# Optimization experiments

Measured on AMD Instinct MI355X. Metric: run time of the kernel, lower is better.

The kernel has to match this reference:

```python
import jax, jax.numpy as jnp
import numpy as np

HID = 64; H = 2; D = 32; L = 2; G = 64; F_IN = 771
NA = 120000; NE = 60000; E0 = 1500000; E1 = 1000000; E2 = 1000000


def _seg_mean(x, seg, n):
    s = jax.ops.segment_sum(x, seg, num_segments=n)
    c = jax.ops.segment_sum(jnp.ones((x.shape[0], 1), x.dtype), seg, num_segments=n)
    return s / jnp.maximum(c, 1.0)


def setup_inputs() -> dict:
    ks = jax.random.split(jax.random.key(0), 32)
    r = lambda i, s: 0.02 * jax.random.normal(ks[i], s, jnp.float32)
    z = lambda s: jnp.zeros(s, jnp.float32)
    inp = {}
    inp['x_argument'] = jax.random.normal(ks[0], (NA, F_IN), jnp.float32)
    inp['x_evidence'] = jax.random.normal(ks[1], (NE, F_IN), jnp.float32)
    inp['Win'] = r(2, (2, F_IN, HID)); inp['b_in'] = z((2, HID))
    inp['Wk'] = r(3, (L, 2, HID, HID)); inp['bk'] = z((L, 2, HID))
    inp['Wq'] = r(4, (L, 2, HID, HID)); inp['bq'] = z((L, 2, HID))
    inp['Wv'] = r(5, (L, 2, HID, HID)); inp['bv'] = z((L, 2, HID))
    inp['Wa'] = r(6, (L, 2, HID, HID)); inp['ba'] = z((L, 2, HID))
    inp['skip'] = jnp.ones((L, 2), jnp.float32)
    inp['Watt'] = r(7, (L, 3, H, D, D)); inp['Wmsg'] = r(8, (L, 3, H, D, D))
    inp['prel'] = jnp.ones((L, 3, H), jnp.float32)
    inp['Wnews'] = r(9, (384, HID)); inp['bnews'] = z((HID,))
    inp['Wdeb'] = r(10, (HID, HID)); inp['bdeb'] = z((HID,))
    inp['Wqm'] = r(11, (HID, HID)); inp['bqm'] = z((HID,))
    inp['Wkm'] = r(12, (HID, HID)); inp['bkm'] = z((HID,))
    inp['Wvm'] = r(13, (HID, HID)); inp['bvm'] = z((HID,))
    inp['Wom'] = r(14, (HID, HID)); inp['bom'] = z((HID,))
    inp['Wc1'] = r(15, (2 * HID, 64)); inp['bc1'] = z((64,))
    inp['Wc2'] = r(16, (64, 1)); inp['bc2'] = z((1,))
    inp['e0_src'] = jax.random.randint(ks[17], (E0,), 0, NA)
    inp['e0_dst'] = jax.random.randint(ks[18], (E0,), 0, NA)
    inp['e1_src'] = jax.random.randint(ks[19], (E1,), 0, NE)
    inp['e1_dst'] = jax.random.randint(ks[20], (E1,), 0, NA)
    inp['e2_src'] = jax.random.randint(ks[21], (E2,), 0, NA)
    inp['e2_dst'] = jax.random.randint(ks[22], (E2,), 0, NE)
    inp['batch_arg'] = jnp.sort(jax.random.randint(ks[23], (NA,), 0, G))
    return inp


def reference(x_argument, x_evidence, Win, b_in, Wk, bk, Wq, bq, Wv, bv, Wa, ba,
              skip, Watt, Wmsg, prel, Wnews, bnews, Wdeb, bdeb,
              Wqm, bqm, Wkm, bkm, Wvm, bvm, Wom, bom, Wc1, bc1, Wc2, bc2,
              e0_src, e0_dst, e1_src, e1_dst, e2_src, e2_dst, batch_arg):
    # Claim embedding from RAW features (slice 384:768), pooled per graph.
    claim_raw = _seg_mean(x_argument[:, 384:768], batch_arg, G)
    # Per-node-type input projection + ReLU. type 0 = argument, 1 = evidence.
    xs = [jax.nn.relu(x_argument @ Win[0] + b_in[0]),
          jax.nn.relu(x_evidence @ Win[1] + b_in[1])]
    # (src_type, dst_type, src_idx, dst_idx) for each heterogeneous edge type.
    edges = [(0, 0, e0_src, e0_dst), (1, 0, e1_src, e1_dst), (0, 1, e2_src, e2_dst)]
    scale = 1.0 / jnp.sqrt(jnp.float32(D))
    for l in range(L):  # HGTConv stack
        Kt = [(xs[t] @ Wk[l, t] + bk[l, t]).reshape(-1, H, D) for t in range(2)]
        Qt = [(xs[t] @ Wq[l, t] + bq[l, t]).reshape(-1, H, D) for t in range(2)]
        Vt = [(xs[t] @ Wv[l, t] + bv[l, t]).reshape(-1, H, D) for t in range(2)]
        buf = {0: [], 1: []}
        for e, (s, d, src, dst) in enumerate(edges):
            k2 = jnp.einsum('ehd,hdf->ehf', Kt[s][src], Watt[l, e])  # relation key transform
            v2 = jnp.einsum('ehd,hdf->ehf', Vt[s][src], Wmsg[l, e])  # relation msg transform
            sc = (Qt[d][dst] * k2).sum(-1) * prel[l, e] * scale      # (E, H)
            buf[d].append((sc, dst, v2))
        new_xs = []
        for d in range(2):
            n = xs[d].shape[0]
            sc = jnp.concatenate([b[0] for b in buf[d]], 0)
            dst = jnp.concatenate([b[1] for b in buf[d]], 0)
            v2 = jnp.concatenate([b[2] for b in buf[d]], 0)
            # segment softmax over all incoming edges of each destination node
            m = jax.ops.segment_max(sc, dst, num_segments=n)
            ex = jnp.exp(sc - m[dst])
            den = jax.ops.segment_sum(ex, dst, num_segments=n)
            alpha = ex / den[dst]
            agg = jax.ops.segment_sum(alpha[..., None] * v2, dst, num_segments=n).reshape(n, HID)
            out = jax.nn.gelu(agg, approximate=False) @ Wa[l, d] + ba[l, d]
            beta = jax.nn.sigmoid(skip[l, d])
            new_xs.append(beta * out + (1.0 - beta) * xs[d])
        xs = new_xs
    graph_emb = _seg_mean(xs[0], batch_arg, G)
    eF = claim_raw @ Wnews + bnews          # (G, HID)
    g = graph_emb @ Wdeb + bdeb             # (G, HID)
    # MultiheadAttention with query len 1 and key len 1: softmax over a single
    # key is identically 1, so attn_out == out_proj(v_proj(g)) exactly
    # (Wqm/bqm/Wkm/bkm receive exactly zero gradient, matching torch).
    v = g @ Wvm + bvm
    attn_out = v @ Wom + bom
    h = jax.nn.relu(jnp.concatenate([g, attn_out], -1) @ Wc1 + bc1)  # dropout is eval-mode identity
    return h @ Wc2 + bc2  # (G, 1)
```

## Files before the change

### kernel.cpp

```cpp
#include <hip/hip_runtime.h>
#include <math.h>

#define N0 120000
#define N1 60000
#define E0N 1500000
#define E1N 1000000
#define E2N 1000000
#define FIN 771
#define NG 64
#define KSTEPS_IN 25

#define GB0 ((N0 + 127) / 128)
#define GB1 ((N1 + 127) / 128)
#define AB0 ((N0 + 3) / 4)
#define AB1 ((N1 + 3) / 4)
#define SB0 ((N0 + 1023) / 1024)
#define SB1 ((N1 + 1023) / 1024)

#define Q0O   ((size_t)0)
#define KV00O ((size_t)N0 * 64)
#define KV02O ((size_t)N0 * 192)
#define Q1O   ((size_t)N0 * 320)
#define KV11O ((size_t)N0 * 320 + (size_t)N1 * 64)

typedef __attribute__((ext_vector_type(8))) short short8;
typedef __attribute__((ext_vector_type(4))) float f32x4;
typedef float f32x4u __attribute__((ext_vector_type(4), aligned(4)));
typedef __attribute__((ext_vector_type(4))) unsigned short ushort4v;
typedef unsigned short ushort;

__device__ __forceinline__ float gelu_f(float v) {
    return 0.5f * v * (1.f + erff(v * 0.70710678118654752f));
}
__device__ __forceinline__ ushort f2b(float f) {
    union { float f; unsigned u; } v; v.f = f;
    unsigned u = v.u;
    return (ushort)((u + 0x7FFFu + ((u >> 16) & 1u)) >> 16);
}
__device__ __forceinline__ float lo16(unsigned u) {
    union { unsigned x; float f; } v; v.x = u << 16; return v.f;
}
__device__ __forceinline__ float hi16(unsigned u) {
    union { unsigned x; float f; } v; v.x = u & 0xFFFF0000u; return v.f;
}
__device__ __forceinline__ int asi(float f) { union { float f; int i; } v; v.f = f; return v.i; }
__device__ __forceinline__ float asf(int i) { union { int i; float f; } v; v.i = i; return v.f; }

__global__ __launch_bounds__(256) void in_proj_all(
    const float* __restrict__ xa, const float* __restrict__ xe,
    const ushort* __restrict__ Wpin, const float* __restrict__ b_in,
    float* __restrict__ xs0, float* __restrict__ xs1)
{
    const int bx = blockIdx.x;
    const int type = (bx >= GB0) ? 1 : 0;
    const float* __restrict__ x = type ? xe : xa;
    const int nrows = type ? N1 : N0;
    const ushort* __restrict__ Wp = Wpin + (type ? (size_t)KSTEPS_IN * 2048 : 0);
    const float* __restrict__ bias = b_in + type * 64;
    float* __restrict__ out = type ? xs1 : xs0;

    const int tid = threadIdx.x, w = tid >> 6, lane = tid & 63;
    const int r0 = (type ? bx - GB0 : bx) * 128 + w * 32;

    const int rA = min(r0 + (lane & 15), nrows - 1);
    const int rB = min(r0 + 16 + (lane & 15), nrows - 1);
    const float* __restrict__ xA = x + (size_t)rA * FIN + (lane >> 4) * 8;
    const float* __restrict__ xB = x + (size_t)rB * FIN + (lane >> 4) * 8;

    f32x4 acc[2][4] = {};
    f32x4u cA0 = *(const f32x4u*)xA;
    f32x4u cA1 = *(const f32x4u*)(xA + 4);
    f32x4u cB0 = *(const f32x4u*)xB;
    f32x4u cB1 = *(const f32x4u*)(xB + 4);

    for (int ks = 0; ks < 24; ++ks) {
        f32x4u nA0 = {}, nA1 = {}, nB0 = {}, nB1 = {};
        if (ks < 23) {
            const float* pA = xA + (ks + 1) * 32;
            const float* pB = xB + (ks + 1) * 32;
            nA0 = *(const f32x4u*)pA; nA1 = *(const f32x4u*)(pA + 4);
            nB0 = *(const f32x4u*)pB; nB1 = *(const f32x4u*)(pB + 4);
        }
        short8 bA, bB;
        #pragma unroll
        for (int j = 0; j < 4; ++j) {
            bA[j]     = (short)f2b(cA0[j]);
            bA[j + 4] = (short)f2b(cA1[j]);
            bB[j]     = (short)f2b(cB0[j]);
            bB[j + 4] = (short)f2b(cB1[j]);
        }
        const ushort* wb = Wp + (size_t)ks * 2048 + lane * 8;
        #pragma unroll
        for (int cg = 0; cg < 4; ++cg) {
            short8 afr = *(const short8*)&wb[cg * 512];
            acc[0][cg] = __builtin_amdgcn_mfma_f32_16x16x32_bf16(afr, bA, acc[0][cg], 0, 0, 0);
            acc[1][cg] = __builtin_amdgcn_mfma_f32_16x16x32_bf16(afr, bB, acc[1][cg], 0, 0, 0);
        }
        cA0 = nA0; cA1 = nA1; cB0 = nB0; cB1 = nB1;
    }
    {
        short8 bA = {}, bB = {};
        if ((lane >> 4) == 0) {
            const float* tA = x + (size_t)rA * FIN + 768;
            const float* tB = x + (size_t)rB * FIN + 768;
            bA[0] = (short)f2b(tA[0]); bA[1] = (short)f2b(tA[1]); bA[2] = (short)f2b(tA[2]);
            bB[0] = (short)f2b(tB[0]); bB[1] = (short)f2b(tB[1]); bB[2] = (short)f2b(tB[2]);
        }
        const ushort* wb = Wp + (size_t)24 * 2048 + lane * 8;
        #pragma unroll
        for (int cg = 0; cg < 4; ++cg) {
            short8 afr = *(const short8*)&wb[cg * 512];
            acc[0][cg] = __builtin_amdgcn_mfma_f32_16x16x32_bf16(afr, bA, acc[0][cg], 0, 0, 0);
            acc[1][cg] = __builtin_amdgcn_mfma_f32_16x16x32_bf16(afr, bB, acc[1][cg], 0, 0, 0);
        }
    }
    const int c0b = (lane >> 4) * 4;
    #pragma unroll
    for (int rb = 0; rb < 2; ++rb) {
        int r = r0 + rb * 16 + (lane & 15);
        if (r < nrows) {
            #pragma unroll
            for (int cg = 0; cg < 4; ++cg) {
                int c = cg * 16 + c0b;
                float4 o;
                o.x = fmaxf(acc[rb][cg][0] + bias[c + 0], 0.f);
                o.y = fmaxf(acc[rb][cg][1] + bias[c + 1], 0.f);
                o.z = fmaxf(acc[rb][cg][2] + bias[c + 2], 0.f);
                o.w = fmaxf(acc[rb][cg][3] + bias[c + 3], 0.f);
                *(float4*)&out[(size_t)r * 64 + c] = o;
            }
        }
    }
}

__global__ __launch_bounds__(256) void proj_fused(
    const float* __restrict__ xs0, const float* __restrict__ xs1,
    const ushort* __restrict__ Wpack, const float* __restrict__ bpack,
    ushort* __restrict__ projAll, int l)
{
    const int bx = blockIdx.x;
    const int type = (bx >= GB0) ? 1 : 0;
    const float* __restrict__ in = type ? xs1 : xs0;
    const int nrows = type ? N1 : N0;
    const int tid = threadIdx.x, w = tid >> 6, lane = tid & 63;
    const int r0 = (type ? bx - GB0 : bx) * 128 + w * 32;

    short8 bfr[2][2];
    #pragma unroll
    for (int ksp = 0; ksp < 2; ++ksp) {
        #pragma unroll
        for (int rb = 0; rb < 2; ++rb) {
            int gr = min(r0 + rb * 16 + (lane & 15), nrows - 1);
            const float* src = in + (size_t)gr * 64 + ksp * 32 + (lane >> 4) * 8;
            float4 f0 = *(const float4*)src;
            float4 f1 = *(const float4*)(src + 4);
            short8 t;
            t[0] = (short)f2b(f0.x); t[1] = (short)f2b(f0.y);
            t[2] = (short)f2b(f0.z); t[3] = (short)f2b(f0.w);
            t[4] = (short)f2b(f1.x); t[5] = (short)f2b(f1.y);
            t[6] = (short)f2b(f1.z); t[7] = (short)f2b(f1.w);
            bfr[ksp][rb] = t;
        }
    }

    const int nslots = type ? 3 : 5;
    const int sbase = l * 8 + (type ? 5 : 0);
    const int c0b = (lane >> 4) * 4;

    for (int slot = 0; slot < nslots; ++slot) {
        const ushort* Wp = Wpack + (size_t)(sbase + slot) * 4096;
        const float* bias = bpack + (size_t)(sbase + slot) * 64;
        size_t ooff; unsigned pitch, qs, ph;
        if (slot == 0) { ooff = type ? Q1O : Q0O; pitch = 64; qs = 4; ph = 0; }
        else {
            int kv = (slot + 1) >> 1;
            ooff = type ? KV11O : (kv == 1 ? KV00O : KV02O);
            pitch = 128; qs = 8; ph = (slot & 1) ? 0u : 4u;
        }
        ushort* out = projAll + ooff;
        f32x4 acc[2][4] = {};
        #pragma unroll
        for (int ksp = 0; ksp < 2; ++ksp) {
            const ushort* wb = Wp + ksp * 2048 + lane * 8;
            #pragma unroll
            for (int cg = 0; cg < 4; ++cg) {
                short8 afr = *(const short8*)&wb[cg * 512];
                acc[0][cg] = __builtin_amdgcn_mfma_f32_16x16x32_bf16(afr, bfr[ksp][0], acc[0][cg], 0, 0, 0);
                acc[1][cg] = __builtin_amdgcn_mfma_f32_16x16x32_bf16(afr, bfr[ksp][1], acc[1][cg], 0, 0, 0);
            }
        }
        #pragma unroll
        for (int rb = 0; rb < 2; ++rb) {
            int r = r0 + rb * 16 + (lane & 15);
            if (r < nrows) {
                #pragma unroll
                for (int cg = 0; cg < 4; ++cg) {
                    int c = cg * 16 + c0b;
                    ushort4v o;
                    o[0] = f2b(acc[rb][cg][0] + bias[c + 0]);
                    o[1] = f2b(acc[rb][cg][1] + bias[c + 1]);
                    o[2] = f2b(acc[rb][cg][2] + bias[c + 2]);
                    o[3] = f2b(acc[rb][cg][3] + bias[c + 3]);
                    *(ushort4v*)&out[(size_t)r * pitch + (unsigned)(c >> 2) * qs + ph] = o;
                }
            }
        }
    }
}

__global__ __launch_bounds__(256) void epi_fused(
    const float* __restrict__ agg0, const float* __restrict__ agg1,
    const ushort* __restrict__ WaPack, const float* __restrict__ ba,
    float* __restrict__ xs0, float* __restrict__ xs1,
    const float* __restrict__ skip, int l)
{
    const int bx = blockIdx.x;
    const int type = (bx >= GB0) ? 1 : 0;
    const float* __restrict__ in = type ? agg1 : agg0;
    float* __restrict__ xs = type ? xs1 : xs0;
    const int nrows = type ? N1 : N0;
    const ushort* __restrict__ Wp = WaPack + (size_t)(l * 2 + type) * 4096;
    const float* __restrict__ bias = ba + (size_t)(l * 2 + type) * 64;
    const float beta = 1.f / (1.f + __expf(-skip[l * 2 + type]));

    const int tid = threadIdx.x, w = tid >> 6, lane = tid & 63;
    const int r0 = (type ? bx - GB0 : bx) * 128 + w * 32;
    f32x4 acc[2][4] = {};
    #pragma unroll
    for (int ksp = 0; ksp < 2; ++ksp) {
        short8 bfr[2];
        #pragma unroll
        for (int rb = 0; rb < 2; ++rb) {
            int gr = min(r0 + rb * 16 + (lane & 15), nrows - 1);
            const float* src = in + (size_t)gr * 64 + ksp * 32 + (lane >> 4) * 8;
            float4 f0 = *(const float4*)src;
            float4 f1 = *(const float4*)(src + 4);
            short8 t;
            t[0] = (short)f2b(gelu_f(f0.x)); t[1] = (short)f2b(gelu_f(f0.y));
            t[2] = (short)f2b(gelu_f(f0.z)); t[3] = (short)f2b(gelu_f(f0.w));
            t[4] = (short)f2b(gelu_f(f1.x)); t[5] = (short)f2b(gelu_f(f1.y));
            t[6] = (short)f2b(gelu_f(f1.z)); t[7] = (short)f2b(gelu_f(f1.w));
            bfr[rb] = t;
        }
        const ushort* wb = Wp + ksp * 2048 + lane * 8;
        #pragma unroll
        for (int cg = 0; cg < 4; ++cg) {
            short8 afr = *(const short8*)&wb[cg * 512];
            acc[0][cg] = __builtin_amdgcn_mfma_f32_16x16x32_bf16(afr, bfr[0], acc[0][cg], 0, 0, 0);
            acc[1][cg] = __builtin_amdgcn_mfma_f32_16x16x32_bf16(afr, bfr[1], acc[1][cg], 0, 0, 0);
        }
    }
    const int c0b = (lane >> 4) * 4;
    #pragma unroll
    for (int rb = 0; rb < 2; ++rb) {
        int r = r0 + rb * 16 + (lane & 15);
        if (r < nrows) {
            #pragma unroll
            for (int cg = 0; cg < 4; ++cg) {
                int c = cg * 16 + c0b;
                float4 xo = *(const float4*)&xs[(size_t)r * 64 + c];
                float4 o;
                o.x = beta * (acc[rb][cg][0] + bias[c + 0]) + (1.f - beta) * xo.x;
                o.y = beta * (acc[rb][cg][1] + bias[c + 1]) + (1.f - beta) * xo.y;
                o.z = beta * (acc[rb][cg][2] + bias[c + 2]) + (1.f - beta) * xo.z;
                o.w = beta * (acc[rb][cg][3] + bias[c + 3]) + (1.f - beta) * xo.w;
                *(float4*)&xs[(size_t)r * 64 + c] = o;
            }
        }
    }
}

__global__ __launch_bounds__(256) void prep_kernel(
    const float* __restrict__ Wq, const float* __restrict__ bq,
    const float* __restrict__ Wk, const float* __restrict__ bk,
    const float* __restrict__ Wv, const float* __restrict__ bv,
    const float* __restrict__ Watt, const float* __restrict__ Wmsg,
    const float* __restrict__ prel, const float* __restrict__ Win,
    const float* __restrict__ Wa,
    ushort* __restrict__ Wpack, float* __restrict__ bpack,
    ushort* __restrict__ Wpin, ushort* __restrict__ WaPack)
{
    __shared__ float WF[4096];
    const int b = blockIdx.x;
    const int tid = threadIdx.x;
    if (b < 16) {
        const int l = b >> 3;
        const int slot = b & 7;
        const float SCALE = 0.17677669529663689f;
        ushort* outW = Wpack + (size_t)(l * 8 + slot) * 4096;
        float* outB = bpack + (size_t)(l * 8 + slot) * 64;
        const float *Wsrc = 0, *bsrc = 0, *A = 0, *prelE = 0;
        int copy = 0;
        switch (slot) {
            case 0: Wsrc = Wq + (l*2+0)*4096; bsrc = bq + (l*2+0)*64; copy = 1; break;
            case 5: Wsrc = Wq + (l*2+1)*4096; bsrc = bq + (l*2+1)*64; copy = 1; break;
            case 1: Wsrc = Wk + (l*2+0)*4096; bsrc = bk + (l*2+0)*64; A = Watt + (l*3+0)*2048; prelE = prel + l*6 + 0; break;
            case 2: Wsrc = Wv + (l*2+0)*4096; bsrc = bv + (l*2+0)*64; A = Wmsg + (l*3+0)*2048; break;
            case 3: Wsrc = Wk + (l*2+0)*4096; bsrc = bk + (l*2+0)*64; A = Watt + (l*3+2)*2048; prelE = prel + l*6 + 4; break;
            case 4: Wsrc = Wv + (l*2+0)*4096; bsrc = bv + (l*2+0)*64; A = Wmsg + (l*3+2)*2048; break;
            case 6: Wsrc = Wk + (l*2+1)*4096; bsrc = bk + (l*2+1)*64; A = Watt + (l*3+1)*2048; prelE = prel + l*6 + 2; break;
            case 7: Wsrc = Wv + (l*2+1)*4096; bsrc = bv + (l*2+1)*64; A = Wmsg + (l*3+1)*2048; break;
        }
        if (copy) {
            for (int idx = tid; idx < 4096; idx += 256) WF[idx] = Wsrc[idx];
            if (tid < 64) outB[tid] = bsrc[tid];
        } else {
            for (int idx = tid; idx < 4096; idx += 256) {
                int k = idx >> 6, c = idx & 63, h = c >> 5, f = c & 31;
                float s = 0.f;
                for (int d = 0; d < 32; ++d)
                    s += Wsrc[k * 64 + h * 32 + d] * A[(h * 32 + d) * 32 + f];
                if (prelE) s *= prelE[h] * SCALE;
                WF[idx] = s;
            }
            if (tid < 64) {
                int h = tid >> 5, f = tid & 31;
                float s = 0.f;
                for (int d = 0; d < 32; ++d)
                    s += bsrc[h * 32 + d] * A[(h * 32 + d) * 32 + f];
                if (prelE) s *= prelE[h] * SCALE;
                outB[tid] = s;
            }
        }
        __syncthreads();
        for (int idx = tid; idx < 4096; idx += 256) {
            int ksp = idx >> 11, rem = idx & 2047;
            int cg = rem >> 9, rem2 = rem & 511;
            int lane = rem2 >> 3, j = rem2 & 7;
            int k = ksp * 32 + (lane >> 4) * 8 + j;
            int c = cg * 16 + (lane & 15);
            outW[idx] = f2b(WF[k * 64 + c]);
        }
    } else if (b < 16 + 2 * KSTEPS_IN) {
        const int pb = b - 16;
        const int type = pb / KSTEPS_IN, ks = pb % KSTEPS_IN;
        const float* W = Win + (size_t)type * FIN * 64;
        ushort* out = Wpin + (size_t)pb * 2048;
        for (int idx = tid; idx < 2048; idx += 256) {
            int cg = idx >> 9, rem = idx & 511, lane = rem >> 3, j = rem & 7;
            int k = ks * 32 + (lane >> 4) * 8 + j;
            int c = cg * 16 + (lane & 15);
            out[idx] = f2b((k < FIN) ? W[(size_t)k * 64 + c] : 0.f);
        }
    } else {
        const int mb = b - 16 - 2 * KSTEPS_IN;
        const float* W = Wa + (size_t)mb * 4096;
        ushort* o = WaPack + (size_t)mb * 4096;
        for (int idx = tid; idx < 4096; idx += 256) {
            int ksp = idx >> 11, rem = idx & 2047;
            int cg = rem >> 9, rem2 = rem & 511;
            int lane = rem2 >> 3, j = rem2 & 7;
            int k = ksp * 32 + (lane >> 4) * 8 + j;
            int c = cg * 16 + (lane & 15);
            o[idx] = f2b(W[k * 64 + c]);
        }
    }
}

__global__ void zero4_kernel(int* __restrict__ c0, int* __restrict__ c1,
                             int* __restrict__ gs, int* __restrict__ gc)
{
    int i = blockIdx.x * blockDim.x + threadIdx.x;
    if (i < N0) c0[i] = 0;
    else if (i < N0 + N1) c1[i - N0] = 0;
    else if (i < N0 + N1 + NG * 64) gs[i - N0 - N1] = 0;
    else if (i < N0 + N1 + NG * 64 + NG) gc[i - N0 - N1 - NG * 64] = 0;
}

__global__ void hist_all_kernel(
    const int* __restrict__ e0d, const int* __restrict__ e1d, const int* __restrict__ e2d,
    int* __restrict__ cnt0, int* __restrict__ cnt1)
{
    const int total = E0N + E1N + E2N;
    for (int i = blockIdx.x * blockDim.x + threadIdx.x; i < total; i += gridDim.x * blockDim.x) {
        if (i < E0N) atomicAdd(&cnt0[e0d[i]], 1);
        else if (i < E0N + E1N) atomicAdd(&cnt0[e1d[i - E0N]], 1);
        else atomicAdd(&cnt1[e2d[i - E0N - E1N]], 1);
    }
}

__global__ __launch_bounds__(256) void scan1_all_kernel(
    int* __restrict__ cnt0, int* __restrict__ cnt1,
    int* __restrict__ off0, int* __restrict__ off1,
    int* __restrict__ bsA, int* __restrict__ bsB)
{
    __shared__ int sa[256], sb[256];
    const int tid = threadIdx.x;
    const int b = blockIdx.x;
    int* cnt; int n; int* off; int* bsum; int lb;
    if (b < SB0) { cnt = cnt0; n = N0; off = off0; bsum = bsA; lb = b; }
    else { cnt = cnt1; n = N1; off = off1; bsum = bsB; lb = b - SB0; }
    const int base = lb * 1024 + tid * 4;
    int v[4];
    int run = 0;
    #pragma unroll
    for (int i = 0; i < 4; ++i) {
        int x = (base + i < n) ? cnt[base + i] : 0;
        run += x; v[i] = run;
    }
    #pragma unroll
    for (int i = 0; i < 4; ++i)
        if (base + i < n) cnt[base + i] = 0;
    sa[tid] = run;
    __syncthreads();
    int* src = sa; int* dst = sb;
    for (int d = 1; d < 256; d <<= 1) {
        int x = src[tid];
        if (tid >= d) x += src[tid - d];
        dst[tid] = x;
        __syncthreads();
        int* t = src; src = dst; dst = t;
    }
    int excl = src[tid] - run;
    #pragma unroll
    for (int i = 0; i < 4; ++i)
        if (base + i < n) off[base + i + 1] = excl + v[i];
    if (tid == 255) bsum[lb] = src[255];
}

__global__ __launch_bounds__(256) void scan2_all_kernel(int* __restrict__ bsA, int* __restrict__ bsB)
{
    __shared__ int sa[256], sb[256];
    const int tid = threadIdx.x;
    int* bsum = blockIdx.x ? bsB : bsA;
    const int nb = blockIdx.x ? SB1 : SB0;
    int x = (tid < nb) ? bsum[tid] : 0;
    sa[tid] = x;
    __syncthreads();
    int* src = sa; int* dst = sb;
    for (int d = 1; d < 256; d <<= 1) {
        int y = src[tid];
        if (tid >= d) y += src[tid - d];
        dst[tid] = y;
        __syncthreads();
        int* t = src; src = dst; dst = t;
    }
    if (tid < nb) bsum[tid] = src[tid] - x;
}

__global__ __launch_bounds__(256) void scan3_all_kernel(
    int* __restrict__ off0, int* __restrict__ off1,
    const int* __restrict__ bsA, const int* __restrict__ bsB)
{
    const int b = blockIdx.x;
    int* off; const int* boff; int n; int lb;
    if (b < SB0) { off = off0; boff = bsA; n = N0; lb = b; }
    else { off = off1; boff = bsB; n = N1; lb = b - SB0; }
    const int base = lb * 1024 + threadIdx.x * 4;
    const int add = boff[lb];
    #pragma unroll
    for (int i = 0; i < 4; ++i)
        if (base + i < n) off[base + i + 1] += add;
    if (lb == 0 && threadIdx.x == 0) off[0] = 0;
}

__global__ void scatter_all_kernel(
    const int* __restrict__ e0s, const int* __restrict__ e0d,
    const int* __restrict__ e1s, const int* __restrict__ e1d,
    const int* __restrict__ e2s, const int* __restrict__ e2d,
    const int* __restrict__ off0, const int* __restrict__ off1,
    int* __restrict__ cnt0, int* __restrict__ cnt1,
    int* __restrict__ rec0, int* __restrict__ rec1)
{
    const int total = E0N + E1N + E2N;
    for (int i = blockIdx.x * blockDim.x + threadIdx.x; i < total; i += gridDim.x * blockDim.x) {
        if (i < E0N) {
            int d = e0d[i];
            int pos = off0[d] + atomicAdd(&cnt0[d], 1);
            rec0[pos] = e0s[i];
        } else if (i < E0N + E1N) {
            int k = i - E0N;
            int d = e1d[k];
            int pos = off0[d] + atomicAdd(&cnt0[d], 1);
            rec0[pos] = e1s[k] | (1 << 20);
        } else {
            int k = i - E0N - E1N;
            int d = e2d[k];
            int pos = off1[d] + atomicAdd(&cnt1[d], 1);
            rec1[pos] = e2s[k];
        }
    }
}

__global__ __launch_bounds__(256) void agg_fused(
    const int* __restrict__ off0, const int* __restrict__ rec0,
    const int* __restrict__ off1, const int* __restrict__ rec1,
    const ushort* __restrict__ projAll,
    float* __restrict__ agg0, float* __restrict__ agg1)
{
    const int bx = blockIdx.x;
    const int type = (bx >= AB0) ? 1 : 0;
    const int lane = threadIdx.x & 63;
    const int node = (type ? bx - AB0 : bx) * 4 + (threadIdx.x >> 6);
    const int ndst = type ? N1 : N0;
    if (node >= ndst) return;
    const int* __restrict__ off = type ? off1 : off0;
    const int* __restrict__ rec = type ? rec1 : rec0;
    const ushort* __restrict__ Q   = projAll + (type ? Q1O : Q0O);
    const ushort* __restrict__ KVa = projAll + (type ? KV02O : KV00O);
    const ushort* __restrict__ KVb = projAll + (type ? KV02O : KV11O);
    float* __restrict__ outAgg = type ? agg1 : agg0;

    const int grp = lane >> 4;
    const int gi  = lane & 15;
    float q0, q1, q2, q3;
    {
        const unsigned* qp = (const unsigned*)(Q + (size_t)node * 64 + gi * 4);
        unsigned u0 = qp[0], u1 = qp[1];
        q0 = lo16(u0); q1 = hi16(u0); q2 = lo16(u1); q3 = hi16(u1);
    }
    const int s = off[node], e = off[node + 1];
    float den = 0.f, a0 = 0.f, a1 = 0.f, a2 = 0.f, a3 = 0.f;
    for (int j = s; j < e; j += 8) {
        int jj0 = j + grp, jj1 = jj0 + 4;
        bool v0 = jj0 < e, v1 = jj1 < e;
        int r0 = rec[v0 ? jj0 : s];
        int r1 = rec[v1 ? jj1 : s];
        const ushort* KV0 = (r0 & (1 << 20)) ? KVb : KVa;
        const ushort* KV1 = (r1 & (1 << 20)) ? KVb : KVa;
        uint4 kv0 = *(const uint4*)(KV0 + ((size_t)(unsigned)(r0 & 0xFFFFF) << 7) + gi * 8);
        uint4 kv1 = *(const uint4*)(KV1 + ((size_t)(unsigned)(r1 & 0xFFFFF) << 7) + gi * 8);
        float p0 = lo16(kv0.x) * q0 + hi16(kv0.x) * q1 + lo16(kv0.y) * q2 + hi16(kv0.y) * q3;
        float p1 = lo16(kv1.x) * q0 + hi16(kv1.x) * q1 + lo16(kv1.y) * q2 + hi16(kv1.y) * q3;
        p0 += asf(__builtin_amdgcn_ds_swizzle(asi(p0), 0x041F));
        p1 += asf(__builtin_amdgcn_ds_swizzle(asi(p1), 0x041F));
        p0 += asf(__builtin_amdgcn_ds_swizzle(asi(p0), 0x081F));
        p1 += asf(__builtin_amdgcn_ds_swizzle(asi(p1), 0x081F));
        p0 += asf(__builtin_amdgcn_ds_swizzle(asi(p0), 0x101F));
        p1 += asf(__builtin_amdgcn_ds_swizzle(asi(p1), 0x101F));
        float w0 = v0 ? __expf(p0) : 0.f;
        float w1 = v1 ? __expf(p1) : 0.f;
        den += w0 + w1;
        a0 = fmaf(w0, lo16(kv0.z), a0); a0 = fmaf(w1, lo16(kv1.z), a0);
        a1 = fmaf(w0, hi16(kv0.z), a1); a1 = fmaf(w1, hi16(kv1.z), a1);
        a2 = fmaf(w0, lo16(kv0.w), a2); a2 = fmaf(w1, lo16(kv1.w), a2);
        a3 = fmaf(w0, hi16(kv0.w), a3); a3 = fmaf(w1, hi16(kv1.w), a3);
    }
    a0 += __shfl_xor(a0, 16); a0 += __shfl_xor(a0, 32);
    a1 += __shfl_xor(a1, 16); a1 += __shfl_xor(a1, 32);
    a2 += __shfl_xor(a2, 16); a2 += __shfl_xor(a2, 32);
    a3 += __shfl_xor(a3, 16); a3 += __shfl_xor(a3, 32);
    den += __shfl_xor(den, 16); den += __shfl_xor(den, 32);
    if (lane < 16) {
        float inv = (den > 0.f) ? 1.f / den : 0.f;
        float4 o;
        o.x = a0 * inv; o.y = a1 * inv; o.z = a2 * inv; o.w = a3 * inv;
        *(float4*)&outAgg[(size_t)node * 64 + gi * 4] = o;
    }
}

__global__ __launch_bounds__(256) void segsum_kernel(
    const float* __restrict__ xs, const int* __restrict__ seg, int n,
    float* __restrict__ gsum, int* __restrict__ gcnt)
{
    const int lane = threadIdx.x & 63;
    const int wid = blockIdx.x * 4 + (threadIdx.x >> 6);
    const int rbeg = wid * 256;
    if (rbeg >= n) return;
    const int rend = min(rbeg + 256, n);
    float s = 0.f;
    int cur = seg[rbeg];
    int run = 0;
    for (int r = rbeg; r < rend; ++r) {
        int sg = seg[r];
        if (sg != cur) {
            atomicAdd(&gsum[cur * 64 + lane], s);
            if (lane == 0) atomicAdd(&gcnt[cur], run);
            cur = sg; s = 0.f; run = 0;
        }
        s += xs[(size_t)r * 64 + lane];
        run++;
    }
    atomicAdd(&gsum[cur * 64 + lane], s);
    if (lane == 0) atomicAdd(&gcnt[cur], run);
}

__global__ __launch_bounds__(256) void head_kernel(
    const float* __restrict__ gsum, const int* __restrict__ gcnt,
    const float* __restrict__ Wdeb, const float* __restrict__ bdeb,
    const float* __restrict__ Wvm, const float* __restrict__ bvm,
    const float* __restrict__ Wom, const float* __restrict__ bom,
    const float* __restrict__ Wc1, const float* __restrict__ bc1,
    const float* __restrict__ Wc2, const float* __restrict__ bc2,
    float* __restrict__ outp)
{
    __shared__ float A[4096], B[4096], C[4096];
    const int tid = threadIdx.x;
    for (int idx = tid; idx < 4096; idx += 256) {
        int g = idx >> 6;
        A[idx] = gsum[idx] / fmaxf((float)gcnt[g], 1.f);
    }
    __syncthreads();
    for (int idx = tid; idx < 4096; idx += 256) {
        int g = idx >> 6, c = idx & 63;
        float s = bdeb[c];
        for (int k = 0; k < 64; ++k) s = fmaf(A[g * 64 + k], Wdeb[k * 64 + c], s);
        B[idx] = s;
    }
    __syncthreads();
    for (int idx = tid; idx < 4096; idx += 256) {
        int g = idx >> 6, c = idx & 63;
        float s = bvm[c];
        for (int k = 0; k < 64; ++k) s = fmaf(B[g * 64 + k], Wvm[k * 64 + c], s);
        C[idx] = s;
    }
    __syncthreads();
    for (int idx = tid; idx < 4096; idx += 256) {
        int g = idx >> 6, c = idx & 63;
        float s = bom[c];
        for (int k = 0; k < 64; ++k) s = fmaf(C[g * 64 + k], Wom[k * 64 + c], s);
        A[idx] = s;
    }
    __syncthreads();
    for (int idx = tid; idx < 4096; idx += 256) {
        int g = idx >> 6, c = idx & 63;
        float s = bc1[c];
        for (int k = 0; k < 64; ++k) s = fmaf(B[g * 64 + k], Wc1[k * 64 + c], s);
        for (int k = 0; k < 64; ++k) s = fmaf(A[g * 64 + k], Wc1[(64 + k) * 64 + c], s);
        C[idx] = fmaxf(s, 0.f);
    }
    __syncthreads();
    if (tid < 64) {
        float s = bc2[0];
        for (int c = 0; c < 64; ++c) s = fmaf(C[tid * 64 + c], Wc2[c], s);
        outp[tid] = s;
    }
}

extern "C" void kernel_launch(void* const* d_in, const int* in_sizes, int n_in,
                              void* d_out, int out_size, void* d_ws, size_t ws_size,
                              hipStream_t stream)
{
    const float* x_arg = (const float*)d_in[0];
    const float* x_ev  = (const float*)d_in[1];
    const float* Win   = (const float*)d_in[2];
    const float* b_in  = (const float*)d_in[3];
    const float* Wk    = (const float*)d_in[4];
    const float* bk    = (const float*)d_in[5];
    const float* Wq    = (const float*)d_in[6];
    const float* bq    = (const float*)d_in[7];
    const float* Wv    = (const float*)d_in[8];
    const float* bv    = (const float*)d_in[9];
    const float* Wa    = (const float*)d_in[10];
    const float* ba    = (const float*)d_in[11];
    const float* skip  = (const float*)d_in[12];
    const float* Watt  = (const float*)d_in[13];
    const float* Wmsg  = (const float*)d_in[14];
    const float* prel  = (const float*)d_in[15];
    const float* Wdeb  = (const float*)d_in[18];
    const float* bdeb  = (const float*)d_in[19];
    const float* Wvm   = (const float*)d_in[24];
    const float* bvm   = (const float*)d_in[25];
    const float* Wom   = (const float*)d_in[26];
    const float* bom   = (const float*)d_in[27];
    const float* Wc1   = (const float*)d_in[28];
    const float* bc1   = (const float*)d_in[29];
    const float* Wc2   = (const float*)d_in[30];
    const float* bc2   = (const float*)d_in[31];
    const int* e0s = (const int*)d_in[32];
    const int* e0d = (const int*)d_in[33];
    const int* e1s = (const int*)d_in[34];
    const int* e1d = (const int*)d_in[35];
    const int* e2s = (const int*)d_in[36];
    const int* e2d = (const int*)d_in[37];
    const int* batch = (const int*)d_in[38];
    float* outp = (float*)d_out;

    char* w = (char*)d_ws;
    size_t o = 0;
    auto alloc = [&](size_t bytes) -> char* {
        char* p = w + o;
        o = (o + bytes + 255) & ~(size_t)255;
        return p;
    };
    float* xs0   = (float*)alloc((size_t)N0 * 64 * 4);
    float* xs1   = (float*)alloc((size_t)N1 * 64 * 4);
    ushort* projAll = (ushort*)alloc(((size_t)N0 * 320 + (size_t)N1 * 192) * 2);
    float* agg0  = (float*)alloc((size_t)N0 * 64 * 4);
    float* agg1  = (float*)alloc((size_t)N1 * 64 * 4);
    int* off0 = (int*)alloc((size_t)(N0 + 1) * 4);
    int* off1 = (int*)alloc((size_t)(N1 + 1) * 4);
    int* cnt0 = (int*)alloc((size_t)N0 * 4);
    int* cnt1 = (int*)alloc((size_t)N1 * 4);
    int* rec0 = (int*)alloc((size_t)(E0N + E1N) * 4);
    int* rec1 = (int*)alloc((size_t)E2N * 4);
    int* bsA  = (int*)alloc(256 * 4);
    int* bsB  = (int*)alloc(256 * 4);
    ushort* Wpack = (ushort*)alloc((size_t)16 * 4096 * 2);
    float* bpack = (float*)alloc((size_t)16 * 64 * 4);
    ushort* Wpin = (ushort*)alloc((size_t)2 * KSTEPS_IN * 2048 * 2);
    ushort* WaPack = (ushort*)alloc((size_t)4 * 4096 * 2);
    float* gsum = (float*)alloc((size_t)NG * 64 * 4);
    int* gcnt = (int*)alloc((size_t)NG * 4);
    if (o > ws_size) return;

    prep_kernel<<<16 + 2 * KSTEPS_IN + 4, 256, 0, stream>>>(
        Wq, bq, Wk, bk, Wv, bv, Watt, Wmsg, prel, Win, Wa, Wpack, bpack, Wpin, WaPack);
    zero4_kernel<<<(N0 + N1 + NG * 64 + NG + 255) / 256, 256, 0, stream>>>(
        cnt0, cnt1, (int*)gsum, gcnt);
    hist_all_kernel<<<2048, 256, 0, stream>>>(e0d, e1d, e2d, cnt0, cnt1);
    scan1_all_kernel<<<SB0 + SB1, 256, 0, stream>>>(cnt0, cnt1, off0, off1, bsA, bsB);
    scan2_all_kernel<<<2, 256, 0, stream>>>(bsA, bsB);
    scan3_all_kernel<<<SB0 + SB1, 256, 0, stream>>>(off0, off1, bsA, bsB);
    scatter_all_kernel<<<2048, 256, 0, stream>>>(
        e0s, e0d, e1s, e1d, e2s, e2d, off0, off1, cnt0, cnt1, rec0, rec1);
    in_proj_all<<<GB0 + GB1, 256, 0, stream>>>(x_arg, x_ev, Wpin, b_in, xs0, xs1);
    for (int l = 0; l < 2; ++l) {
        proj_fused<<<GB0 + GB1, 256, 0, stream>>>(xs0, xs1, Wpack, bpack, projAll, l);
        agg_fused<<<AB0 + AB1, 256, 0, stream>>>(off0, rec0, off1, rec1, projAll, agg0, agg1);
        epi_fused<<<GB0 + GB1, 256, 0, stream>>>(agg0, agg1, WaPack, ba, xs0, xs1, skip, l);
    }
    {
        int waves = (N0 + 255) / 256;
        segsum_kernel<<<(waves + 3) / 4, 256, 0, stream>>>(xs0, batch, N0, gsum, gcnt);
    }
    head_kernel<<<1, 256, 0, stream>>>(gsum, gcnt, Wdeb, bdeb, Wvm, bvm, Wom, bom,
                                       Wc1, bc1, Wc2, bc2, outp);
}
```

Measured before the change: 1.063 ms.

## Fuse projections into input-projection and epilogue kernels, merge scatter with in-proj

```diff
diff --git a/kernel.cpp b/kernel.cpp
--- a/kernel.cpp
+++ b/kernel.cpp
@@ -16,6 +16,8 @@
 #define AB1 ((N1 + 3) / 4)
 #define SB0 ((N0 + 1023) / 1024)
 #define SB1 ((N1 + 1023) / 1024)
+#define PREPB 70
+#define SCB 1024
 
 #define Q0O   ((size_t)0)
 #define KV00O ((size_t)N0 * 64)
@@ -46,123 +48,18 @@
 __device__ __forceinline__ int asi(float f) { union { float f; int i; } v; v.f = f; return v.i; }
 __device__ __forceinline__ float asf(int i) { union { int i; float f; } v; v.i = i; return v.f; }
 
-__global__ __launch_bounds__(256) void in_proj_all(
-    const float* __restrict__ xa, const float* __restrict__ xe,
-    const ushort* __restrict__ Wpin, const float* __restrict__ b_in,
-    float* __restrict__ xs0, float* __restrict__ xs1)
-{
-    const int bx = blockIdx.x;
-    const int type = (bx >= GB0) ? 1 : 0;
-    const float* __restrict__ x = type ? xe : xa;
-    const int nrows = type ? N1 : N0;
-    const ushort* __restrict__ Wp = Wpin + (type ? (size_t)KSTEPS_IN * 2048 : 0);
-    const float* __restrict__ bias = b_in + type * 64;
-    float* __restrict__ out = type ? xs1 : xs0;
-
-    const int tid = threadIdx.x, w = tid >> 6, lane = tid & 63;
-    const int r0 = (type ? bx - GB0 : bx) * 128 + w * 32;
-
-    const int rA = min(r0 + (lane & 15), nrows - 1);
-    const int rB = min(r0 + 16 + (lane & 15), nrows - 1);
-    const float* __restrict__ xA = x + (size_t)rA * FIN + (lane >> 4) * 8;
-    const float* __restrict__ xB = x + (size_t)rB * FIN + (lane >> 4) * 8;
-
-    f32x4 acc[2][4] = {};
-    f32x4u cA0 = *(const f32x4u*)xA;
-    f32x4u cA1 = *(const f32x4u*)(xA + 4);
-    f32x4u cB0 = *(const f32x4u*)xB;
-    f32x4u cB1 = *(const f32x4u*)(xB + 4);
-
-    for (int ks = 0; ks < 24; ++ks) {
-        f32x4u nA0 = {}, nA1 = {}, nB0 = {}, nB1 = {};
-        if (ks < 23) {
-            const float* pA = xA + (ks + 1) * 32;
-            const float* pB = xB + (ks + 1) * 32;
-            nA0 = *(const f32x4u*)pA; nA1 = *(const f32x4u*)(pA + 4);
-            nB0 = *(const f32x4u*)pB; nB1 = *(const f32x4u*)(pB + 4);
-        }
-        short8 bA, bB;
-        #pragma unroll
-        for (int j = 0; j < 4; ++j) {
-            bA[j]     = (short)f2b(cA0[j]);
-            bA[j + 4] = (short)f2b(cA1[j]);
-            bB[j]     = (short)f2b(cB0[j]);
-            bB[j + 4] = (short)f2b(cB1[j]);
-        }
-        const ushort* wb = Wp + (size_t)ks * 2048 + lane * 8;
-        #pragma unroll
-        for (int cg = 0; cg < 4; ++cg) {
-            short8 afr = *(const short8*)&wb[cg * 512];
-            acc[0][cg] = __builtin_amdgcn_mfma_f32_16x16x32_bf16(afr, bA, acc[0][cg], 0, 0, 0);
-            acc[1][cg] = __builtin_amdgcn_mfma_f32_16x16x32_bf16(afr, bB, acc[1][cg], 0, 0, 0);
-        }
-        cA0 = nA0; cA1 = nA1; cB0 = nB0; cB1 = nB1;
-    }
-    {
-        short8 bA = {}, bB = {};
-        if ((lane >> 4) == 0) {
-            const float* tA = x + (size_t)rA * FIN + 768;
-            const float* tB = x + (size_t)rB * FIN + 768;
-            bA[0] = (short)f2b(tA[0]); bA[1] = (short)f2b(tA[1]); bA[2] = (short)f2b(tA[2]);
-            bB[0] = (short)f2b(tB[0]); bB[1] = (short)f2b(tB[1]); bB[2] = (short)f2b(tB[2]);
-        }
-        const ushort* wb = Wp + (size_t)24 * 2048 + lane * 8;
-        #pragma unroll
-        for (int cg = 0; cg < 4; ++cg) {
-            short8 afr = *(const short8*)&wb[cg * 512];
-            acc[0][cg] = __builtin_amdgcn_mfma_f32_16x16x32_bf16(afr, bA, acc[0][cg], 0, 0, 0);
-            acc[1][cg] = __builtin_amdgcn_mfma_f32_16x16x32_bf16(afr, bB, acc[1][cg], 0, 0, 0);
-        }
-    }
-    const int c0b = (lane >> 4) * 4;
-    #pragma unroll
-    for (int rb = 0; rb < 2; ++rb) {
-        int r = r0 + rb * 16 + (lane & 15);
-        if (r < nrows) {
-            #pragma unroll
-            for (int cg = 0; cg < 4; ++cg) {
-                int c = cg * 16 + c0b;
-                float4 o;
-                o.x = fmaxf(acc[rb][cg][0] + bias[c + 0], 0.f);
-                o.y = fmaxf(acc[rb][cg][1] + bias[c + 1], 0.f);
-                o.z = fmaxf(acc[rb][cg][2] + bias[c + 2], 0.f);
-                o.w = fmaxf(acc[rb][cg][3] + bias[c + 3], 0.f);
-                *(float4*)&out[(size_t)r * 64 + c] = o;
-            }
-        }
-    }
-}
-
-__global__ __launch_bounds__(256) void proj_fused(
-    const float* __restrict__ xs0, const float* __restrict__ xs1,
+__device__ __forceinline__ void proj_phase(
+    const ushort* xls, int type, int l, int w, int lane, int r0, int nrows,
     const ushort* __restrict__ Wpack, const float* __restrict__ bpack,
-    ushort* __restrict__ projAll, int l)
-{
-    const int bx = blockIdx.x;
-    const int type = (bx >= GB0) ? 1 : 0;
-    const float* __restrict__ in = type ? xs1 : xs0;
-    const int nrows = type ? N1 : N0;
-    const int tid = threadIdx.x, w = tid >> 6, lane = tid & 63;
-    const int r0 = (type ? bx - GB0 : bx) * 128 + w * 32;
-
+    ushort* __restrict__ projAll)
+{
     short8 bfr[2][2];
     #pragma unroll
-    for (int ksp = 0; ksp < 2; ++ksp) {
-        #pragma unroll
-        for (int rb = 0; rb < 2; ++rb) {
-            int gr = min(r0 + rb * 16 + (lane & 15), nrows - 1);
-            const float* src = in + (size_t)gr * 64 + ksp * 32 + (lane >> 4) * 8;
-            float4 f0 = *(const float4*)src;
-            float4 f1 = *(const float4*)(src + 4);
-            short8 t;
-            t[0] = (short)f2b(f0.x); t[1] = (short)f2b(f0.y);
-            t[2] = (short)f2b(f0.z); t[3] = (short)f2b(f0.w);
-            t[4] = (short)f2b(f1.x); t[5] = (short)f2b(f1.y);
-            t[6] = (short)f2b(f1.z); t[7] = (short)f2b(f1.w);
-            bfr[ksp][rb] = t;
-        }
-    }
-
+    for (int ksp = 0; ksp < 2; ++ksp)
+        #pragma unroll
+        for (int rb = 0; rb < 2; ++rb)
+            bfr[ksp][rb] = *(const short8*)&xls[(w * 32 + rb * 16 + (lane & 15)) * 72
+                                                + ksp * 32 + (lane >> 4) * 8];
     const int nslots = type ? 3 : 5;
     const int sbase = l * 8 + (type ? 5 : 0);
     const int c0b = (lane >> 4) * 4;
@@ -208,12 +105,141 @@
     }
 }
 
-__global__ __launch_bounds__(256) void epi_fused(
+__global__ __launch_bounds__(256) void scatter_inproj_kernel(
+    const int* __restrict__ e0s, const int* __restrict__ e0d,
+    const int* __restrict__ e1s, const int* __restrict__ e1d,
+    const int* __restrict__ e2s, const int* __restrict__ e2d,
+    const int* __restrict__ off0, const int* __restrict__ off1,
+    int* __restrict__ cnt0, int* __restrict__ cnt1,
+    int* __restrict__ rec0, int* __restrict__ rec1,
+    const float* __restrict__ xa, const float* __restrict__ xe,
+    const ushort* __restrict__ Wpin, const float* __restrict__ b_in,
+    float* __restrict__ xs0, float* __restrict__ xs1,
+    const ushort* __restrict__ Wpack, const float* __restrict__ bpack,
+    ushort* __restrict__ projAll)
+{
+    __shared__ ushort xls[128 * 72];
+    if (blockIdx.x < SCB) {
+        const int total = E0N + E1N + E2N;
+        for (int i = blockIdx.x * 256 + threadIdx.x; i < total; i += SCB * 256) {
+            if (i < E0N) {
+                int d = e0d[i];
+                int pos = off0[d] + atomicAdd(&cnt0[d], 1);
+                rec0[pos] = e0s[i];
+            } else if (i < E0N + E1N) {
+                int k = i - E0N;
+                int d = e1d[k];
+                int pos = off0[d] + atomicAdd(&cnt0[d], 1);
+                rec0[pos] = e1s[k] | (1 << 20);
+            } else {
+                int k = i - E0N - E1N;
+                int d = e2d[k];
+                int pos = off1[d] + atomicAdd(&cnt1[d], 1);
+                rec1[pos] = e2s[k];
+            }
+        }
+        return;
+    }
+    const int bx = blockIdx.x - SCB;
+    const int type = (bx >= GB0) ? 1 : 0;
+    const float* __restrict__ x = type ? xe : xa;
+    const int nrows = type ? N1 : N0;
+    const ushort* __restrict__ Wp = Wpin + (type ? (size_t)KSTEPS_IN * 2048 : 0);
+    const float* __restrict__ bias = b_in + type * 64;
+    float* __restrict__ out = type ? xs1 : xs0;
+
+    const int tid = threadIdx.x, w = tid >> 6, lane = tid & 63;
+    const int r0b = (type ? bx - GB0 : bx) * 128;
+    const int r0 = r0b + w * 32;
+
+    const int rA = min(r0 + (lane & 15), nrows - 1);
+    const int rB = min(r0 + 16 + (lane & 15), nrows - 1);
+    const float* __restrict__ xA = x + (size_t)rA * FIN + (lane >> 4) * 8;
+    const float* __restrict__ xB = x + (size_t)rB * FIN + (lane >> 4) * 8;
+
+    f32x4 acc[2][4] = {};
+    f32x4u cb[3][4];
+    cb[0][0] = *(const f32x4u*)xA;       cb[0][1] = *(const f32x4u*)(xA + 4);
+    cb[0][2] = *(const f32x4u*)xB;       cb[0][3] = *(const f32x4u*)(xB + 4);
+    cb[1][0] = *(const f32x4u*)(xA + 32); cb[1][1] = *(const f32x4u*)(xA + 36);
+    cb[1][2] = *(const f32x4u*)(xB + 32); cb[1][3] = *(const f32x4u*)(xB + 36);
+
+    #pragma unroll
+    for (int ks = 0; ks < 24; ++ks) {
+        if (ks + 2 < 24) {
+            const float* pA = xA + (ks + 2) * 32;
+            const float* pB = xB + (ks + 2) * 32;
+            cb[(ks + 2) % 3][0] = *(const f32x4u*)pA;
+            cb[(ks + 2) % 3][1] = *(const f32x4u*)(pA + 4);
+            cb[(ks + 2) % 3][2] = *(const f32x4u*)pB;
+            cb[(ks + 2) % 3][3] = *(const f32x4u*)(pB + 4);
+        }
+        const int cur = ks % 3;
+        short8 bA, bB;
+        #pragma unroll
+        for (int j = 0; j < 4; ++j) {
+            bA[j]     = (short)f2b(cb[cur][0][j]);
+            bA[j + 4] = (short)f2b(cb[cur][1][j]);
+            bB[j]     = (short)f2b(cb[cur][2][j]);
+            bB[j + 4] = (short)f2b(cb[cur][3][j]);
+        }
+        const ushort* wb = Wp + (size_t)ks * 2048 + lane * 8;
+        #pragma unroll
+        for (int cg = 0; cg < 4; ++cg) {
+            short8 afr = *(const short8*)&wb[cg * 512];
+            acc[0][cg] = __builtin_amdgcn_mfma_f32_16x16x32_bf16(afr, bA, acc[0][cg], 0, 0, 0);
+            acc[1][cg] = __builtin_amdgcn_mfma_f32_16x16x32_bf16(afr, bB, acc[1][cg], 0, 0, 0);
+        }
+    }
+    {
+        short8 bA = {}, bB = {};
+        if ((lane >> 4) == 0) {
+            const float* tA = x + (size_t)rA * FIN + 768;
+            const float* tB = x + (size_t)rB * FIN + 768;
+            bA[0] = (short)f2b(tA[0]); bA[1] = (short)f2b(tA[1]); bA[2] = (short)f2b(tA[2]);
+            bB[0] = (short)f2b(tB[0]); bB[1] = (short)f2b(tB[1]); bB[2] = (short)f2b(tB[2]);
+        }
+        const ushort* wb = Wp + (size_t)24 * 2048 + lane * 8;
+        #pragma unroll
+        for (int cg = 0; cg < 4; ++cg) {
+            short8 afr = *(const short8*)&wb[cg * 512];
+            acc[0][cg] = __builtin_amdgcn_mfma_f32_16x16x32_bf16(afr, bA, acc[0][cg], 0, 0, 0);
+            acc[1][cg] = __builtin_amdgcn_mfma_f32_16x16x32_bf16(afr, bB, acc[1][cg], 0, 0, 0);
+        }
+    }
+    const int c0b = (lane >> 4) * 4;
+    #pragma unroll
+    for (int rb = 0; rb < 2; ++rb) {
+        int lrow = w * 32 + rb * 16 + (lane & 15);
+        int r = r0b + lrow;
+        #pragma unroll
+        for (int cg = 0; cg < 4; ++cg) {
+            int c = cg * 16 + c0b;
+            float4 o;
+            o.x = fmaxf(acc[rb][cg][0] + bias[c + 0], 0.f);
+            o.y = fmaxf(acc[rb][cg][1] + bias[c + 1], 0.f);
+            o.z = fmaxf(acc[rb][cg][2] + bias[c + 2], 0.f);
+            o.w = fmaxf(acc[rb][cg][3] + bias[c + 3], 0.f);
+            ushort4v h;
+            h[0] = f2b(o.x); h[1] = f2b(o.y); h[2] = f2b(o.z); h[3] = f2b(o.w);
+            *(ushort4v*)&xls[lrow * 72 + c] = h;
+            if (r < nrows) *(float4*)&out[(size_t)r * 64 + c] = o;
+        }
+    }
+    __syncthreads();
+    proj_phase(xls, type, 0, w, lane, r0, nrows, Wpack, bpack, projAll);
+}
+
+template <int DO_PROJ>
+__global__ __launch_bounds__(256) void epi_kernel(
     const float* __restrict__ agg0, const float* __restrict__ agg1,
     const ushort* __restrict__ WaPack, const float* __restrict__ ba,
     float* __restrict__ xs0, float* __restrict__ xs1,
-    const float* __restrict__ skip, int l)
-{
+    const float* __restrict__ skip, int l,
+    const ushort* __restrict__ Wpack, const float* __restrict__ bpack,
+    ushort* __restrict__ projAll)
+{
+    __shared__ ushort xls[DO_PROJ ? 128 * 72 : 64];
     const int bx = blockIdx.x;
     const int type = (bx >= GB0) ? 1 : 0;
     const float* __restrict__ in = type ? agg1 : agg0;
@@ -224,7 +250,8 @@
     const float beta = 1.f / (1.f + __expf(-skip[l * 2 + type]));
 
     const int tid = threadIdx.x, w = tid >> 6, lane = tid & 63;
-    const int r0 = (type ? bx - GB0 : bx) * 128 + w * 32;
+    const int r0b = (type ? bx - GB0 : bx) * 128;
+    const int r0 = r0b + w * 32;
     f32x4 acc[2][4] = {};
     #pragma unroll
     for (int ksp = 0; ksp < 2; ++ksp) {
@@ -253,24 +280,33 @@
     const int c0b = (lane >> 4) * 4;
     #pragma unroll
     for (int rb = 0; rb < 2; ++rb) {
-        int r = r0 + rb * 16 + (lane & 15);
-        if (r < nrows) {
-            #pragma unroll
-            for (int cg = 0; cg < 4; ++cg) {
-                int c = cg * 16 + c0b;
-                float4 xo = *(const float4*)&xs[(size_t)r * 64 + c];
-                float4 o;
-                o.x = beta * (acc[rb][cg][0] + bias[c + 0]) + (1.f - beta) * xo.x;
-                o.y = beta * (acc[rb][cg][1] + bias[c + 1]) + (1.f - beta) * xo.y;
-                o.z = beta * (acc[rb][cg][2] + bias[c + 2]) + (1.f - beta) * xo.z;
-                o.w = beta * (acc[rb][cg][3] + bias[c + 3]) + (1.f - beta) * xo.w;
-                *(float4*)&xs[(size_t)r * 64 + c] = o;
+        int lrow = w * 32 + rb * 16 + (lane & 15);
+        int r = r0b + lrow;
+        int gr = min(r, nrows - 1);
+        #pragma unroll
+        for (int cg = 0; cg < 4; ++cg) {
+            int c = cg * 16 + c0b;
+            float4 xo = *(const float4*)&xs[(size_t)gr * 64 + c];
+            float4 o;
+            o.x = beta * (acc[rb][cg][0] + bias[c + 0]) + (1.f - beta) * xo.x;
+            o.y = beta * (acc[rb][cg][1] + bias[c + 1]) + (1.f - beta) * xo.y;
+            o.z = beta * (acc[rb][cg][2] + bias[c + 2]) + (1.f - beta) * xo.z;
+            o.w = beta * (acc[rb][cg][3] + bias[c + 3]) + (1.f - beta) * xo.w;
+            if (DO_PROJ) {
+                ushort4v h;
+                h[0] = f2b(o.x); h[1] = f2b(o.y); h[2] = f2b(o.z); h[3] = f2b(o.w);
+                *(ushort4v*)&xls[lrow * 72 + c] = h;
             }
-        }
-    }
-}
-
-__global__ __launch_bounds__(256) void prep_kernel(
+            if (r < nrows) *(float4*)&xs[(size_t)r * 64 + c] = o;
+        }
+    }
+    if (DO_PROJ) {
+        __syncthreads();
+        proj_phase(xls, type, l + 1, w, lane, r0, nrows, Wpack, bpack, projAll);
+    }
+}
+
+__global__ __launch_bounds__(256) void prep_zero_kernel(
     const float* __restrict__ Wq, const float* __restrict__ bq,
     const float* __restrict__ Wk, const float* __restrict__ bk,
     const float* __restrict__ Wv, const float* __restrict__ bv,
@@ -278,11 +314,21 @@
     const float* __restrict__ prel, const float* __restrict__ Win,
     const float* __restrict__ Wa,
     ushort* __restrict__ Wpack, float* __restrict__ bpack,
-    ushort* __restrict__ Wpin, ushort* __restrict__ WaPack)
+    ushort* __restrict__ Wpin, ushort* __restrict__ WaPack,
+    int* __restrict__ c0, int* __restrict__ c1,
+    int* __restrict__ gs, int* __restrict__ gc)
 {
     __shared__ float WF[4096];
     const int b = blockIdx.x;
     const int tid = threadIdx.x;
+    if (b >= PREPB) {
+        int i = (b - PREPB) * 256 + tid;
+        if (i < N0) c0[i] = 0;
+        else if (i < N0 + N1) c1[i - N0] = 0;
+        else if (i < N0 + N1 + NG * 64) gs[i - N0 - N1] = 0;
+        else if (i < N0 + N1 + NG * 64 + NG) gc[i - N0 - N1 - NG * 64] = 0;
+        return;
+    }
     if (b < 16) {
         const int l = b >> 3;
         const int slot = b & 7;
@@ -357,16 +403,6 @@
     }
 }
 
-__global__ void zero4_kernel(int* __restrict__ c0, int* __restrict__ c1,
-                             int* __restrict__ gs, int* __restrict__ gc)
-{
-    int i = blockIdx.x * blockDim.x + threadIdx.x;
-    if (i < N0) c0[i] = 0;
-    else if (i < N0 + N1) c1[i - N0] = 0;
-    else if (i < N0 + N1 + NG * 64) gs[i - N0 - N1] = 0;
-    else if (i < N0 + N1 + NG * 64 + NG) gc[i - N0 - N1 - NG * 64] = 0;
-}
-
 __global__ void hist_all_kernel(
     const int* __restrict__ e0d, const int* __restrict__ e1d, const int* __restrict__ e2d,
     int* __restrict__ cnt0, int* __restrict__ cnt1)
@@ -452,34 +488,6 @@
     for (int i = 0; i < 4; ++i)
         if (base + i < n) off[base + i + 1] += add;
     if (lb == 0 && threadIdx.x == 0) off[0] = 0;
-}
-
-__global__ void scatter_all_kernel(
-    const int* __restrict__ e0s, const int* __restrict__ e0d,
-    const int* __restrict__ e1s, const int* __restrict__ e1d,
-    const int* __restrict__ e2s, const int* __restrict__ e2d,
-    const int* __restrict__ off0, const int* __restrict__ off1,
-    int* __restrict__ cnt0, int* __restrict__ cnt1,
-    int* __restrict__ rec0, int* __restrict__ rec1)
-{
-    const int total = E0N + E1N + E2N;
-    for (int i = blockIdx.x * blockDim.x + threadIdx.x; i < total; i += gridDim.x * blockDim.x) {
-        if (i < E0N) {
-            int d = e0d[i];
-            int pos = off0[d] + atomicAdd(&cnt0[d], 1);
-            rec0[pos] = e0s[i];
-        } else if (i < E0N + E1N) {
-            int k = i - E0N;
-            int d = e1d[k];
-            int pos = off0[d] + atomicAdd(&cnt0[d], 1);
-            rec0[pos] = e1s[k] | (1 << 20);
-        } else {
-            int k = i - E0N - E1N;
-            int d = e2d[k];
-            int pos = off1[d] + atomicAdd(&cnt1[d], 1);
-            rec1[pos] = e2s[k];
-        }
-    }
 }
 
 __global__ __launch_bounds__(256) void agg_fused(
@@ -694,22 +702,24 @@
     int* gcnt = (int*)alloc((size_t)NG * 4);
     if (o > ws_size) return;
 
-    prep_kernel<<<16 + 2 * KSTEPS_IN + 4, 256, 0, stream>>>(
-        Wq, bq, Wk, bk, Wv, bv, Watt, Wmsg, prel, Win, Wa, Wpack, bpack, Wpin, WaPack);
-    zero4_kernel<<<(N0 + N1 + NG * 64 + NG + 255) / 256, 256, 0, stream>>>(
-        cnt0, cnt1, (int*)gsum, gcnt);
-    hist_all_kernel<<<2048, 256, 0, stream>>>(e0d, e1d, e2d, cnt0, cnt1);
+    const int ZB = (N0 + N1 + NG * 64 + NG + 255) / 256;
+
+    prep_zero_kernel<<<PREPB + ZB, 256, 0, stream>>>(
+        Wq, bq, Wk, bk, Wv, bv, Watt, Wmsg, prel, Win, Wa,
+        Wpack, bpack, Wpin, WaPack, cnt0, cnt1, (int*)gsum, gcnt);
+    hist_all_kernel<<<1280, 256, 0, stream>>>(e0d, e1d, e2d, cnt0, cnt1);
     scan1_all_kernel<<<SB0 + SB1, 256, 0, stream>>>(cnt0, cnt1, off0, off1, bsA, bsB);
     scan2_all_kernel<<<2, 256, 0, stream>>>(bsA, bsB);
     scan3_all_kernel<<<SB0 + SB1, 256, 0, stream>>>(off0, off1, bsA, bsB);
-    scatter_all_kernel<<<2048, 256, 0, stream>>>(
-        e0s, e0d, e1s, e1d, e2s, e2d, off0, off1, cnt0, cnt1, rec0, rec1);
-    in_proj_all<<<GB0 + GB1, 256, 0, stream>>>(x_arg, x_ev, Wpin, b_in, xs0, xs1);
-    for (int l = 0; l < 2; ++l) {
-        proj_fused<<<GB0 + GB1, 256, 0, stream>>>(xs0, xs1, Wpack, bpack, projAll, l);
-        agg_fused<<<AB0 + AB1, 256, 0, stream>>>(off0, rec0, off1, rec1, projAll, agg0, agg1);
-        epi_fused<<<GB0 + GB1, 256, 0, stream>>>(agg0, agg1, WaPack, ba, xs0, xs1, skip, l);
-    }
+    scatter_inproj_kernel<<<SCB + GB0 + GB1, 256, 0, stream>>>(
+        e0s, e0d, e1s, e1d, e2s, e2d, off0, off1, cnt0, cnt1, rec0, rec1,
+        x_arg, x_ev, Wpin, b_in, xs0, xs1, Wpack, bpack, projAll);
+    agg_fused<<<AB0 + AB1, 256, 0, stream>>>(off0, rec0, off1, rec1, projAll, agg0, agg1);
+    epi_kernel<1><<<GB0 + GB1, 256, 0, stream>>>(
+        agg0, agg1, WaPack, ba, xs0, xs1, skip, 0, Wpack, bpack, projAll);
+    agg_fused<<<AB0 + AB1, 256, 0, stream>>>(off0, rec0, off1, rec1, projAll, agg0, agg1);
+    epi_kernel<0><<<GB0 + GB1, 256, 0, stream>>>(
+        agg0, agg1, WaPack, ba, xs0, xs1, skip, 1, Wpack, bpack, projAll);
     {
         int waves = (N0 + 255) / 256;
         segsum_kernel<<<(waves + 3) / 4, 256, 0, stream>>>(xs0, batch, N0, gsum, gcnt);
```

Result: slower. 1.086 ms (+2.2%).
